# Performance work log

Measured on AMD Instinct MI355X. Metric: run time of the kernel, lower is better.

## Reference

```python
import jax, jax.numpy as jnp
import numpy as np

TWO_PI = 2.0 * np.pi
PC_RANGE = (-140.8, -40.0, -3.0, 140.8, 40.0, 1.0)
IOU_THR = 0.1
EPS = 1e-5


def limit_period(val):
    # maps angle to [-pi, pi)
    return val - jnp.floor(val / TWO_PI + 0.5) * TWO_PI


def _cross(u, v):
    return u[..., 0] * v[..., 1] - u[..., 1] * v[..., 0]


def corners_bev(boxes):
    # boxes: [N,7] = (x, y, z, h, w, l, yaw)  (order 'hwl')
    tmpl = jnp.array([[0.5, 0.5], [0.5, -0.5], [-0.5, -0.5], [-0.5, 0.5]], dtype=boxes.dtype)
    lw = jnp.stack([boxes[:, 5], boxes[:, 4]], axis=-1)  # (l, w)
    pts = tmpl[None] * lw[:, None, :]                     # [N,4,2] local frame
    c = jnp.cos(boxes[:, 6])[:, None]
    s = jnp.sin(boxes[:, 6])[:, None]
    gx = pts[..., 0] * c - pts[..., 1] * s + boxes[:, 0:1]
    gy = pts[..., 0] * s + pts[..., 1] * c + boxes[:, 1:2]
    return jnp.stack([gx, gy], axis=-1)                   # [N,4,2]


def rect_inter_area(corners):
    # pairwise rotated-rectangle intersection area via convex-polygon candidate points
    n = corners.shape[0]
    A = corners[:, None]                                  # [N,1,4,2]
    B = corners[None, :]                                  # [1,N,4,2]
    A2 = jnp.roll(corners, -1, axis=1)[:, None]
    B2 = jnp.roll(corners, -1, axis=1)[None, :]
    a1 = A[:, :, :, None, :]
    d1 = (A2 - A)[:, :, :, None, :]
    b1 = B[:, :, None, :, :]
    d2 = (B2 - B)[:, :, None, :, :]
    den = _cross(d1, d2)                                  # [N,N,4,4]
    den_s = jnp.where(jnp.abs(den) > 1e-8, den, 1e-8)
    t = _cross(b1 - a1, d2) / den_s
    u = _cross(b1 - a1, d1) / den_s
    ok = (jnp.abs(den) > 1e-8) & (t >= 0) & (t <= 1) & (u >= 0) & (u <= 1)
    pint = (a1 + t[..., None] * d1).reshape(n, n, 16, 2)  # edge-edge intersections
    ok = ok.reshape(n, n, 16)
    Ab = jnp.broadcast_to(A, (n, n, 4, 2))
    Bb = jnp.broadcast_to(B, (n, n, 4, 2))
    A2b = jnp.broadcast_to(A2, (n, n, 4, 2))
    B2b = jnp.broadcast_to(B2, (n, n, 4, 2))

    def in_quad(p, q, qn):
        c = _cross(qn[..., None, :, :] - q[..., None, :, :], p[..., :, None, :] - q[..., None, :, :])
        return jnp.all(c <= EPS, -1) | jnp.all(c >= -EPS, -1)

    a_in_b = in_quad(Ab, Bb, B2b)
    b_in_a = in_quad(Bb, Ab, A2b)
    cand = jnp.concatenate([pint, Ab, Bb], axis=2)        # [N,N,24,2]
    m = jnp.concatenate([ok, a_in_b, b_in_a], axis=2)     # [N,N,24]
    cntf = m.sum(-1).astype(cand.dtype)
    cen = (cand * m[..., None]).sum(2) / jnp.maximum(cntf, 1.0)[..., None]
    rel = jnp.where(m[..., None], cand - cen[..., None, :], 0.0)
    ang = jnp.where(m, jnp.arctan2(rel[..., 1], rel[..., 0]), 1e9)
    idx = jnp.argsort(ang, axis=-1)
    rel_s = jnp.take_along_axis(rel, idx[..., None], axis=2)
    m_s = jnp.take_along_axis(m, idx, axis=2)
    rel_s = jnp.where(m_s[..., None], rel_s, rel_s[..., 0:1, :])  # pad with first valid point
    area = 0.5 * jnp.abs(_cross(rel_s, jnp.roll(rel_s, -1, axis=2)).sum(-1))
    return jnp.where(cntf >= 3.0, area, 0.0)


def boxes_iou3d(boxes):
    inter_bev = rect_inter_area(corners_bev(boxes))
    z, h = boxes[:, 2], boxes[:, 3]
    top = z + h / 2
    bot = z - h / 2
    oh = jnp.maximum(jnp.minimum(top[:, None], top[None, :]) - jnp.maximum(bot[:, None], bot[None, :]), 0.0)
    inter = inter_bev * oh
    vol = boxes[:, 3] * boxes[:, 4] * boxes[:, 5]
    return inter / jnp.maximum(vol[:, None] + vol[None, :] - inter, 1e-6)


def clustering(ious):
    # sequential connected-component style clustering exactly as the torch while-loop
    n = ious.shape[0]

    def cond(st):
        return jnp.any(st[0] == 0)

    def body(st):
        ci, cid = st
        idx = jnp.argmax(ci == 0)  # first unassigned box
        ci = jnp.where(ious[idx] > IOU_THR, cid, ci)
        return (ci, cid + 1)

    ci, _ = jax.lax.while_loop(cond, body, (jnp.zeros(n, jnp.int32), jnp.int32(1)))
    return ci


def cluster_fusion(boxes, scores, cids):
    n = boxes.shape[0]
    ns = n + 1  # cluster ids are 1..n; segment 0 unused
    seg_sum = lambda x: jax.ops.segment_sum(x, cids, num_segments=ns)
    cnt = seg_sum(jnp.ones(n, boxes.dtype))
    smax = jax.ops.segment_max(scores, cids, num_segments=ns)
    is_max = scores == smax[cids]
    dirs = boxes[:, 6]
    dref = jax.ops.segment_max(jnp.where(is_max, dirs, -1e9), cids, num_segments=ns)[cids]
    diff = jnp.abs(dirs - dref)
    diff = jnp.where(diff > np.pi, TWO_PI - diff, diff)
    gt = diff > np.pi / 2
    s_lt = seg_sum(jnp.where(gt, scores, 0.0))
    s_le = seg_sum(jnp.where(gt, 0.0, scores))
    keep_major = (s_lt <= s_le)[cids]
    flip = jnp.where(keep_major, gt, ~gt)
    dirs = limit_period(dirs + np.pi * flip.astype(dirs.dtype))
    sn = scores / seg_sum(scores)[cids]
    theta = jnp.arctan2(seg_sum(jnp.sin(dirs) * sn), seg_sum(jnp.cos(dirs) * sn))
    cdim = jax.ops.segment_sum(boxes[:, :6] * sn[:, None], cids, num_segments=ns)
    boxes_f = jnp.concatenate([cdim, theta[:, None]], axis=-1)[1:]
    valid = cnt[1:] > 0
    scores_f = jnp.where(valid, smax[1:], 0.0)
    boxes_f = jnp.where(valid[:, None], boxes_f, 0.0)
    return boxes_f, scores_f, valid


def range_mask(boxes_f):
    c = corners_bev(boxes_f)
    inb = ((c[..., 0] > PC_RANGE[0]) & (c[..., 0] < PC_RANGE[3]) &
           (c[..., 1] > PC_RANGE[1]) & (c[..., 1] < PC_RANGE[4]))
    return jnp.all(inb, axis=-1)


def setup_inputs() -> dict:
    key = jax.random.key(0)
    ks = jax.random.split(key, 8)
    M, D = 128, 4  # 128 objects seen by ~4 agents -> clusters of ~4
    x = jax.random.uniform(ks[0], (M,), minval=-90.0, maxval=90.0)
    y = jax.random.uniform(ks[1], (M,), minval=-30.0, maxval=30.0)
    z = jax.random.uniform(ks[2], (M,), minval=-2.2, maxval=-0.8)
    h = jax.random.uniform(ks[3], (M,), minval=1.4, maxval=1.9)
    w = jax.random.uniform(ks[4], (M,), minval=1.6, maxval=2.2)
    l = jax.random.uniform(ks[5], (M,), minval=3.5, maxval=5.0)
    yaw = jax.random.uniform(ks[6], (M,), minval=-np.pi, maxval=np.pi)
    base = jnp.stack([x, y, z, h, w, l, yaw], axis=-1)
    boxes = jnp.tile(base, (D, 1))
    noise = jax.random.normal(ks[7], (M * D, 7)) * jnp.array([0.3, 0.3, 0.1, 0.05, 0.05, 0.1, 0.05])
    boxes = (boxes + noise).astype(jnp.float32)
    scores = jax.random.uniform(jax.random.fold_in(key, 1), (M * D,), minval=0.1, maxval=1.0).astype(jnp.float32)
    return {"det_boxes": boxes, "det_scores": scores, "feat_h": 100, "feat_w": 352}


def reference(det_boxes, det_scores, feat_h, feat_w):
    boxes = det_boxes.at[:, 6].set(limit_period(det_boxes[:, 6]))
    ious = boxes_iou3d(boxes)
    cids = clustering(ious)
    boxes_f, scores_f, valid = cluster_fusion(boxes, det_scores, cids)
    valid = valid & range_mask(boxes_f)
    boxes_f = jnp.where(valid[:, None], boxes_f, 0.0)
    scores_f = jnp.where(valid, scores_f, 0.0)
    # get_roi_from_box
    gh = (PC_RANGE[4] - PC_RANGE[1]) / feat_h
    gw = (PC_RANGE[3] - PC_RANGE[0]) / feat_w
    gcx = (boxes_f[:, 0] - PC_RANGE[0]) / gw
    gcy = (boxes_f[:, 1] - PC_RANGE[1]) / gh
    gox = boxes_f[:, 5] / 2.0 / gw  # enlarge_ratio = 1
    goy = boxes_f[:, 4] / 2.0 / gh + 1.0
    xmin = jnp.maximum(gcx - gox, 0.0)
    xmax = jnp.minimum(gcx + gox, feat_w - 1.0)
    ymin = jnp.maximum(gcy - goy, 0.0)
    ymax = jnp.minimum(gcy + goy, feat_h - 1.0)
    roi = jnp.stack([xmin, xmax, ymin, ymax], axis=-1).astype(jnp.int32)
    roi = jnp.where(valid[:, None], roi, 0)
    return boxes_f, scores_f, valid, roi
```

## Files before the change

### kernel.cpp

```cpp
#include <hip/hip_runtime.h>

#define N 512
#define ADJW (N/64)
#define MAXC 64
typedef unsigned long long ull;

__device__ __forceinline__ float limit_period_f(float v){
    const float TWO_PI_F = 6.2831853071795864769f;
    return v - floorf(v/TWO_PI_F + 0.5f)*TWO_PI_F;
}

__device__ __forceinline__ unsigned fkey(float f){
    unsigned u = __float_as_uint(f);
    return (u & 0x80000000u) ? ~u : (u | 0x80000000u);
}
__device__ __forceinline__ float fdec(unsigned k){
    unsigned u = (k & 0x80000000u) ? (k ^ 0x80000000u) : ~k;
    return __uint_as_float(u);
}

__global__ __launch_bounds__(512) void adj_kernel(const float* __restrict__ boxes,
                                                  ull* __restrict__ adj){
    int i = blockIdx.x;
    int t = threadIdx.x;
    int l = t & 63, wv = t >> 6;
    int h  = l >> 5;
    int sl = l & 31;
    int hb = wv*2 + h;

    __shared__ int      s_wcnt[8];
    __shared__ int      s_list[MAXC];
    __shared__ unsigned s_row[ADJW*2];
    __shared__ float    s_boxes[N][7];
    __shared__ float    s_px[16][24], s_py[16][24], s_ang[16][24];
    __shared__ float    s_rx[16][24], s_ry[16][24], s_tm[16][24];

    if(t < ADJW*2) s_row[t] = 0u;

    float bi0=boxes[i*7+0], bi1=boxes[i*7+1], bi2=boxes[i*7+2], bi3=boxes[i*7+3],
          bi4=boxes[i*7+4], bi5=boxes[i*7+5], bi6=boxes[i*7+6];
    int j = t;
    float bj0=boxes[j*7+0], bj1=boxes[j*7+1], bj2=boxes[j*7+2], bj3=boxes[j*7+3],
          bj4=boxes[j*7+4], bj5=boxes[j*7+5], bj6=boxes[j*7+6];
    s_boxes[t][0]=bj0; s_boxes[t][1]=bj1; s_boxes[t][2]=bj2; s_boxes[t][3]=bj3;
    s_boxes[t][4]=bj4; s_boxes[t][5]=bj5; s_boxes[t][6]=bj6;

    float topi = bi2 + bi3*0.5f, boti = bi2 - bi3*0.5f;
    float topj = bj2 + bj3*0.5f, botj = bj2 - bj3*0.5f;
    float ohc = fminf(topi, topj) - fmaxf(boti, botj);
    float dx = bi0 - bj0, dy = bi1 - bj1;
    float ra = 0.5f*sqrtf(bi5*bi5 + bi4*bi4);
    float rb = 0.5f*sqrtf(bj5*bj5 + bj4*bj4);
    float rr = ra + rb + 0.01f;
    bool cand = (dx*dx + dy*dy <= rr*rr) && (ohc > 0.0f);

    ull m = __ballot(cand);
    if(l == 0) s_wcnt[wv] = __popcll(m);
    int prefix = __popcll(m & ((1ull<<l) - 1ull));
    __syncthreads();
    int base = 0, C = 0;
    #pragma unroll
    for(int k=0;k<8;++k){ int c = s_wcnt[k]; if(k < wv) base += c; C += c; }
    if(cand){
        int pos = base + prefix;
        if(pos < MAXC) s_list[pos] = j;
    }
    if(C > MAXC) C = MAXC;
    __syncthreads();

    float voli = bi3*bi4*bi5;
    const float tx[4] = {0.5f, 0.5f, -0.5f, -0.5f};
    const float ty[4] = {0.5f, -0.5f, -0.5f, 0.5f};
    float yawi = limit_period_f(bi6);
    float cA = cosf(yawi), sA = sinf(yawi);
    float axv[4], ayv[4];
    #pragma unroll
    for(int k=0;k<4;++k){
        float px = tx[k]*bi5, py = ty[k]*bi4;
        axv[k] = px*cA - py*sA + bi0;
        ayv[k] = px*sA + py*cA + bi1;
    }

    for(int k = hb; k < C; k += 16){
        int jj = s_list[k];
        float cj0=s_boxes[jj][0], cj1=s_boxes[jj][1], cj2=s_boxes[jj][2],
              cj3=s_boxes[jj][3], cj4=s_boxes[jj][4], cj5=s_boxes[jj][5],
              cj6=s_boxes[jj][6];
        float volj = cj3*cj4*cj5;
        float topj2 = cj2 + cj3*0.5f, botj2 = cj2 - cj3*0.5f;
        float oh = fminf(topi, topj2) - fmaxf(boti, botj2);
        float yawj = limit_period_f(cj6);
        float cB = cosf(yawj), sB = sinf(yawj);
        float bxv[4], byv[4];
        #pragma unroll
        for(int kk=0;kk<4;++kk){
            float qx = tx[kk]*cj5, qy = ty[kk]*cj4;
            bxv[kk] = qx*cB - qy*sB + cj0;
            byv[kk] = qx*sB + qy*cB + cj1;
        }

        const float EPSQ = 1e-5f;
        bool valid = false;
        float px = 0.f, py = 0.f;
        if(sl < 16){
            int e1 = sl >> 2, e2 = sl & 3;
            float a1x=axv[e1], a1y=ayv[e1];
            float d1x=axv[(e1+1)&3]-a1x, d1y=ayv[(e1+1)&3]-a1y;
            float b1x=bxv[e2], b1y=byv[e2];
            float d2x=bxv[(e2+1)&3]-b1x, d2y=byv[(e2+1)&3]-b1y;
            float den = d1x*d2y - d1y*d2x;
            bool okd = fabsf(den) > 1e-8f;
            float dens = okd ? den : 1e-8f;
            float wx = b1x-a1x, wy = b1y-a1y;
            float tt = (wx*d2y - wy*d2x)/dens;
            float uu = (wx*d1y - wy*d1x)/dens;
            valid = okd && (tt>=0.f) && (tt<=1.f) && (uu>=0.f) && (uu<=1.f);
            px = a1x + tt*d1x;
            py = a1y + tt*d1y;
        } else if(sl < 20){
            int kk = sl - 16;
            px = axv[kk]; py = ayv[kk];
            bool le=true, ge=true;
            #pragma unroll
            for(int e=0;e<4;++e){
                float qx=bxv[e], qy=byv[e];
                float ux=bxv[(e+1)&3]-qx, uy=byv[(e+1)&3]-qy;
                float cc = ux*(py-qy) - uy*(px-qx);
                le = le && (cc <= EPSQ);
                ge = ge && (cc >= -EPSQ);
            }
            valid = le || ge;
        } else if(sl < 24){
            int kk = sl - 20;
            px = bxv[kk]; py = byv[kk];
            bool le=true, ge=true;
            #pragma unroll
            for(int e=0;e<4;++e){
                float qx=axv[e], qy=ayv[e];
                float ux=axv[(e+1)&3]-qx, uy=ayv[(e+1)&3]-qy;
                float cc = ux*(py-qy) - uy*(px-qx);
                le = le && (cc <= EPSQ);
                ge = ge && (cc >= -EPSQ);
            }
            valid = le || ge;
        }

        ull bm = __ballot(valid);
        unsigned mh = (unsigned)(bm >> (h*32)) & 0xFFFFFFu;
        int c = __popc(mh);
        float cntf = (float)c;

        if(sl < 24){
            s_px[hb][sl] = valid ? px : 0.f;
            s_py[hb][sl] = valid ? py : 0.f;
        }
        asm volatile("s_waitcnt lgkmcnt(0)" ::: "memory");
        float sx = 0.f, sy = 0.f;
        if(sl == 0){
            #pragma unroll
            for(int kk=0;kk<24;++kk){ sx += s_px[hb][kk]; sy += s_py[hb][kk]; }
        }
        sx = __shfl(sx, l & 32);
        sy = __shfl(sy, l & 32);
        float denomc = fmaxf(cntf, 1.f);
        float cenx = sx/denomc, ceny = sy/denomc;

        float relx = valid ? (px - cenx) : 0.f;
        float rely = valid ? (py - ceny) : 0.f;
        float ang  = valid ? atan2f(rely, relx) : 1e9f;

        if(sl < 24) s_ang[hb][sl] = ang;
        asm volatile("s_waitcnt lgkmcnt(0)" ::: "memory");
        int r = 0;
        if(sl < 24){
            #pragma unroll
            for(int qq=0; qq<24; ++qq){
                float aq = s_ang[hb][qq];
                if(aq < ang) r++;
                else if(aq == ang && qq < sl) r++;
            }
        }

        if(sl < 24){
            s_rx[hb][r] = relx;
            s_ry[hb][r] = rely;
        }
        asm volatile("s_waitcnt lgkmcnt(0)" ::: "memory");
        if(sl < 24){
            int nxt = (r+1 < c) ? (r+1) : 0;
            float nx = s_rx[hb][nxt], ny = s_ry[hb][nxt];
            float tm = (r < c) ? (relx*ny - rely*nx) : 0.f;
            s_tm[hb][r] = tm;
        }
        asm volatile("s_waitcnt lgkmcnt(0)" ::: "memory");

        if(sl == 0){
            float acc = 0.f;
            #pragma unroll
            for(int kk=0;kk<24;++kk) acc += s_tm[hb][kk];
            float area = 0.5f*fabsf(acc);
            float inter_bev = (cntf >= 3.f) ? area : 0.f;
            float inter = inter_bev * oh;
            float iou = inter / fmaxf(voli+volj-inter, 1e-6f);
            if(iou > 0.1f) atomicOr(&s_row[jj>>5], 1u << (jj&31));
        }
    }
    __syncthreads();
    if(t < ADJW) adj[i*ADJW + t] = ((ull*)s_row)[t];
}

__global__ __launch_bounds__(64) void cluster_kernel(const ull* __restrict__ adj,
                                                     int* __restrict__ ci){
    int l = threadIdx.x;
    __shared__ ull s_adj[N*ADJW];
    #pragma unroll
    for(int k=0;k<64;++k) s_adj[k*64 + l] = adj[k*64 + l];
    __syncthreads();
    const unsigned char* ab = (const unsigned char*)s_adj;

    ull cov[8] = {0,0,0,0,0,0,0,0};
    int mc[8]  = {0,0,0,0,0,0,0,0};
    int cid = 1;
    #pragma unroll
    for(int g=0; g<8; ++g){
        ull cg = cov[g];
        while(~cg != 0ull){
            int b = (int)__ffsll(~cg) - 1;
            int seed = g*64 + b;
            unsigned myb = (unsigned)ab[seed*64 + l];
            #pragma unroll
            for(int k=0;k<8;++k) cov[k] |= s_adj[seed*8 + k];
            #pragma unroll
            for(int q=0;q<8;++q){ if((myb>>q)&1u) mc[q] = cid; }
            cid++;
            cg = cov[g];
        }
    }
    #pragma unroll
    for(int q=0;q<8;++q) ci[l*8+q] = mc[q];
}

__global__ __launch_bounds__(512) void fuse_kernel(
        const float* __restrict__ boxes,
        const float* __restrict__ scores,
        const int* __restrict__ ci_g,
        const int* __restrict__ fhp,
        const int* __restrict__ fwp,
        float* __restrict__ out){
    const float PI_F      = 3.14159265358979323846f;
    const float HALF_PI_F = 1.57079632679489662f;
    const float TWO_PI_F  = 6.2831853071795864769f;
    int t = threadIdx.x;

    __shared__ int      s_cnt[N];
    __shared__ unsigned s_smaxk[N];
    __shared__ unsigned s_drefk[N];
    __shared__ float    s_ssum[N];
    __shared__ float    s_slt[N], s_sle[N];
    __shared__ float    s_acc[8][N];

    float b0=boxes[t*7+0], b1=boxes[t*7+1], b2=boxes[t*7+2], b3=boxes[t*7+3],
          b4=boxes[t*7+4], b5=boxes[t*7+5], b6=boxes[t*7+6];
    float dir = limit_period_f(b6);
    float sc  = scores[t];
    int ow = ci_g[t] - 1;
    s_cnt[t] = 0;
    s_smaxk[t] = fkey(-1e30f);
    s_drefk[t] = fkey(-1e9f);
    s_ssum[t] = 0.f;
    s_slt[t] = 0.f;
    s_sle[t] = 0.f;
    #pragma unroll
    for(int k=0;k<8;++k) s_acc[k][t] = 0.f;
    __syncthreads();

    atomicAdd(&s_cnt[ow], 1);
    atomicMax(&s_smaxk[ow], fkey(sc));
    atomicAdd(&s_ssum[ow], sc);
    __syncthreads();

    float smax_b = fdec(s_smaxk[ow]);
    if(sc == smax_b) atomicMax(&s_drefk[ow], fkey(dir));
    __syncthreads();

    float drefb = fdec(s_drefk[ow]);
    float diff = fabsf(dir - drefb);
    diff = (diff > PI_F) ? (TWO_PI_F - diff) : diff;
    bool gt = diff > HALF_PI_F;
    atomicAdd(gt ? &s_slt[ow] : &s_sle[ow], sc);
    __syncthreads();

    {
        bool keep = (s_slt[ow] <= s_sle[ow]);
        bool flip = keep ? gt : !gt;
        float d2 = limit_period_f(dir + (flip ? PI_F : 0.f));
        float sn = sc / s_ssum[ow];
        atomicAdd(&s_acc[0][ow], sinf(d2)*sn);
        atomicAdd(&s_acc[1][ow], cosf(d2)*sn);
        atomicAdd(&s_acc[2][ow], b0*sn);
        atomicAdd(&s_acc[3][ow], b1*sn);
        atomicAdd(&s_acc[4][ow], b2*sn);
        atomicAdd(&s_acc[5][ow], b3*sn);
        atomicAdd(&s_acc[6][ow], b4*sn);
        atomicAdd(&s_acc[7][ow], b5*sn);
    }
    __syncthreads();

    int icnt = s_cnt[t];
    float smax = fdec(s_smaxk[t]);
    float theta = atan2f(s_acc[0][t], s_acc[1][t]);
    bool valid = icnt > 0;
    float bf[7];
    bf[0] = valid ? s_acc[2][t] : 0.f;
    bf[1] = valid ? s_acc[3][t] : 0.f;
    bf[2] = valid ? s_acc[4][t] : 0.f;
    bf[3] = valid ? s_acc[5][t] : 0.f;
    bf[4] = valid ? s_acc[6][t] : 0.f;
    bf[5] = valid ? s_acc[7][t] : 0.f;
    bf[6] = valid ? theta : 0.f;
    {
        float cth=cosf(bf[6]), sth=sinf(bf[6]);
        const float tx[4]={0.5f,0.5f,-0.5f,-0.5f};
        const float ty[4]={0.5f,-0.5f,-0.5f,0.5f};
        bool inb = true;
        #pragma unroll
        for(int k=0;k<4;++k){
            float pxl = tx[k]*bf[5], pyl = ty[k]*bf[4];
            float gx = pxl*cth - pyl*sth + bf[0];
            float gy = pxl*sth + pyl*cth + bf[1];
            inb = inb && (gx > -140.8f) && (gx < 140.8f) && (gy > -40.0f) && (gy < 40.0f);
        }
        valid = valid && inb;
    }
    if(!valid){
        #pragma unroll
        for(int d=0;d<7;++d) bf[d]=0.f;
    }
    float sf = valid ? smax : 0.f;
    int fh = *fhp, fw = *fwp;
    float ghf = (float)((40.0 - (-40.0)) / (double)fh);
    float gwf = (float)((140.8 - (-140.8)) / (double)fw);
    float gcx = (bf[0] + 140.8f) / gwf;
    float gcy = (bf[1] + 40.0f) / ghf;
    float gox = bf[5]*0.5f / gwf;
    float goy = bf[4]*0.5f / ghf + 1.0f;
    float xmin = fmaxf(gcx - gox, 0.f);
    float xmax = fminf(gcx + gox, (float)fw - 1.0f);
    float ymin = fmaxf(gcy - goy, 0.f);
    float ymax = fminf(gcy + goy, (float)fh - 1.0f);
    int r0 = (int)xmin, r1 = (int)xmax, r2 = (int)ymin, r3 = (int)ymax;
    if(!valid){ r0=0; r1=0; r2=0; r3=0; }
    #pragma unroll
    for(int d=0;d<7;++d) out[t*7+d] = bf[d];
    out[N*7 + t] = sf;
    out[N*8 + t] = valid ? 1.f : 0.f;
    out[N*9 + t*4 + 0] = (float)r0;
    out[N*9 + t*4 + 1] = (float)r1;
    out[N*9 + t*4 + 2] = (float)r2;
    out[N*9 + t*4 + 3] = (float)r3;
}

extern "C" void kernel_launch(void* const* d_in, const int* in_sizes, int n_in,
                              void* d_out, int out_size, void* d_ws, size_t ws_size,
                              hipStream_t stream) {
    const float* boxes  = (const float*)d_in[0];
    const float* scores = (const float*)d_in[1];
    const int*   fhp    = (const int*)d_in[2];
    const int*   fwp    = (const int*)d_in[3];
    float* out = (float*)d_out;
    char* ws = (char*)d_ws;
    ull* adj = (ull*)ws;
    int* ci  = (int*)(ws + 32768);

    adj_kernel<<<N, 512, 0, stream>>>(boxes, adj);
    cluster_kernel<<<1, 64, 0, stream>>>(adj, ci);
    fuse_kernel<<<1, 512, 0, stream>>>(boxes, scores, ci, fhp, fwp, out);
}
```

Measured before the change: 39.08 us.

## Fuse adjacency, clustering and fusion kernels into one cooperative kernel

Replaces three kernel launches with a single cooperative kernel of 256 blocks. Each block loops over rows to build the IoU adjacency matrix, then a grid-wide sync hands off to block 0, which runs clustering and fusion from shared memory. Each block also stages all boxes in shared memory once instead of reading them per row. The aim is to remove launch gaps and the global round-trip of cluster ids, at the cost of grid-sync overhead and half as many blocks for the adjacency work.

```diff
diff --git a/kernel.cpp b/kernel.cpp
--- a/kernel.cpp
+++ b/kernel.cpp
@@ -1,4 +1,6 @@
 #include <hip/hip_runtime.h>
+#include <hip/hip_cooperative_groups.h>
+namespace cg = cooperative_groups;
 
 #define N 512
 #define ADJW (N/64)
@@ -9,7 +11,6 @@
     const float TWO_PI_F = 6.2831853071795864769f;
     return v - floorf(v/TWO_PI_F + 0.5f)*TWO_PI_F;
 }
-
 __device__ __forceinline__ unsigned fkey(float f){
     unsigned u = __float_as_uint(f);
     return (u & 0x80000000u) ? ~u : (u | 0x80000000u);
@@ -19,251 +20,262 @@
     return __uint_as_float(u);
 }
 
-__global__ __launch_bounds__(512) void adj_kernel(const float* __restrict__ boxes,
-                                                  ull* __restrict__ adj){
-    int i = blockIdx.x;
+__global__ __launch_bounds__(512, 4) void mega_kernel(
+        const float* __restrict__ boxes,
+        const float* __restrict__ scores,
+        const int* __restrict__ fhp,
+        const int* __restrict__ fwp,
+        ull* __restrict__ adj,
+        float* __restrict__ out){
+    const float PI_F      = 3.14159265358979323846f;
+    const float HALF_PI_F = 1.57079632679489662f;
+    const float TWO_PI_F  = 6.2831853071795864769f;
     int t = threadIdx.x;
     int l = t & 63, wv = t >> 6;
     int h  = l >> 5;
     int sl = l & 31;
     int hb = wv*2 + h;
 
-    __shared__ int      s_wcnt[8];
-    __shared__ int      s_list[MAXC];
-    __shared__ unsigned s_row[ADJW*2];
-    __shared__ float    s_boxes[N][7];
-    __shared__ float    s_px[16][24], s_py[16][24], s_ang[16][24];
-    __shared__ float    s_rx[16][24], s_ry[16][24], s_tm[16][24];
-
-    if(t < ADJW*2) s_row[t] = 0u;
-
-    float bi0=boxes[i*7+0], bi1=boxes[i*7+1], bi2=boxes[i*7+2], bi3=boxes[i*7+3],
-          bi4=boxes[i*7+4], bi5=boxes[i*7+5], bi6=boxes[i*7+6];
-    int j = t;
-    float bj0=boxes[j*7+0], bj1=boxes[j*7+1], bj2=boxes[j*7+2], bj3=boxes[j*7+3],
-          bj4=boxes[j*7+4], bj5=boxes[j*7+5], bj6=boxes[j*7+6];
-    s_boxes[t][0]=bj0; s_boxes[t][1]=bj1; s_boxes[t][2]=bj2; s_boxes[t][3]=bj3;
-    s_boxes[t][4]=bj4; s_boxes[t][5]=bj5; s_boxes[t][6]=bj6;
-
-    float topi = bi2 + bi3*0.5f, boti = bi2 - bi3*0.5f;
-    float topj = bj2 + bj3*0.5f, botj = bj2 - bj3*0.5f;
-    float ohc = fminf(topi, topj) - fmaxf(boti, botj);
-    float dx = bi0 - bj0, dy = bi1 - bj1;
-    float ra = 0.5f*sqrtf(bi5*bi5 + bi4*bi4);
-    float rb = 0.5f*sqrtf(bj5*bj5 + bj4*bj4);
-    float rr = ra + rb + 0.01f;
-    bool cand = (dx*dx + dy*dy <= rr*rr) && (ohc > 0.0f);
-
-    ull m = __ballot(cand);
-    if(l == 0) s_wcnt[wv] = __popcll(m);
-    int prefix = __popcll(m & ((1ull<<l) - 1ull));
-    __syncthreads();
-    int base = 0, C = 0;
+    __shared__ __align__(16) char s_raw[34816];
+    float (*s_boxes)[7] = (float(*)[7])s_raw;
+    int*      p_list = (int*)(s_raw + 14336);
+    unsigned* p_row  = (unsigned*)(s_raw + 14592);
+    int*      p_wcnt = (int*)(s_raw + 14656);
+    float* p_px  = (float*)(s_raw + 14720);
+    float* p_py  = p_px  + 16*24;
+    float* p_ang = p_py  + 16*24;
+    float* p_rx  = p_ang + 16*24;
+    float* p_ry  = p_rx  + 16*24;
+    float* p_tm  = p_ry  + 16*24;
+
     #pragma unroll
-    for(int k=0;k<8;++k){ int c = s_wcnt[k]; if(k < wv) base += c; C += c; }
-    if(cand){
-        int pos = base + prefix;
-        if(pos < MAXC) s_list[pos] = j;
-    }
-    if(C > MAXC) C = MAXC;
-    __syncthreads();
-
-    float voli = bi3*bi4*bi5;
+    for(int d=0; d<7; ++d) s_boxes[t][d] = boxes[t*7+d];
+    __syncthreads();
+
     const float tx[4] = {0.5f, 0.5f, -0.5f, -0.5f};
     const float ty[4] = {0.5f, -0.5f, -0.5f, 0.5f};
-    float yawi = limit_period_f(bi6);
-    float cA = cosf(yawi), sA = sinf(yawi);
-    float axv[4], ayv[4];
+
+    for(int row = blockIdx.x; row < N; row += gridDim.x){
+        __syncthreads();
+        if(t < ADJW*2) p_row[t] = 0u;
+
+        float bi0=s_boxes[row][0], bi1=s_boxes[row][1], bi2=s_boxes[row][2],
+              bi3=s_boxes[row][3], bi4=s_boxes[row][4], bi5=s_boxes[row][5],
+              bi6=s_boxes[row][6];
+        int j = t;
+        float bj0=s_boxes[j][0], bj1=s_boxes[j][1], bj2=s_boxes[j][2],
+              bj3=s_boxes[j][3], bj4=s_boxes[j][4], bj5=s_boxes[j][5];
+
+        float topi = bi2 + bi3*0.5f, boti = bi2 - bi3*0.5f;
+        float topj = bj2 + bj3*0.5f, botj = bj2 - bj3*0.5f;
+        float ohc = fminf(topi, topj) - fmaxf(boti, botj);
+        float dx = bi0 - bj0, dy = bi1 - bj1;
+        float ra = 0.5f*sqrtf(bi5*bi5 + bi4*bi4);
+        float rb = 0.5f*sqrtf(bj5*bj5 + bj4*bj4);
+        float rr = ra + rb + 0.01f;
+        bool cand = (dx*dx + dy*dy <= rr*rr) && (ohc > 0.0f);
+
+        ull m = __ballot(cand);
+        if(l == 0) p_wcnt[wv] = __popcll(m);
+        int prefix = __popcll(m & ((1ull<<l) - 1ull));
+        __syncthreads();
+        int base = 0, C = 0;
+        #pragma unroll
+        for(int k=0;k<8;++k){ int c = p_wcnt[k]; if(k < wv) base += c; C += c; }
+        if(cand){
+            int pos = base + prefix;
+            if(pos < MAXC) p_list[pos] = j;
+        }
+        if(C > MAXC) C = MAXC;
+        __syncthreads();
+
+        float voli = bi3*bi4*bi5;
+        float yawi = limit_period_f(bi6);
+        float cA = cosf(yawi), sA = sinf(yawi);
+        float axv[4], ayv[4];
+        #pragma unroll
+        for(int k=0;k<4;++k){
+            float px = tx[k]*bi5, py = ty[k]*bi4;
+            axv[k] = px*cA - py*sA + bi0;
+            ayv[k] = px*sA + py*cA + bi1;
+        }
+
+        for(int k = hb; k < C; k += 16){
+            int jj = p_list[k];
+            float cj0=s_boxes[jj][0], cj1=s_boxes[jj][1], cj2=s_boxes[jj][2],
+                  cj3=s_boxes[jj][3], cj4=s_boxes[jj][4], cj5=s_boxes[jj][5],
+                  cj6=s_boxes[jj][6];
+            float volj = cj3*cj4*cj5;
+            float topj2 = cj2 + cj3*0.5f, botj2 = cj2 - cj3*0.5f;
+            float oh = fminf(topi, topj2) - fmaxf(boti, botj2);
+            float yawj = limit_period_f(cj6);
+            float cB = cosf(yawj), sB = sinf(yawj);
+            float bxv[4], byv[4];
+            #pragma unroll
+            for(int kk=0;kk<4;++kk){
+                float qx = tx[kk]*cj5, qy = ty[kk]*cj4;
+                bxv[kk] = qx*cB - qy*sB + cj0;
+                byv[kk] = qx*sB + qy*cB + cj1;
+            }
+
+            const float EPSQ = 1e-5f;
+            bool valid = false;
+            float px = 0.f, py = 0.f;
+            if(sl < 16){
+                int e1 = sl >> 2, e2 = sl & 3;
+                float a1x=axv[e1], a1y=ayv[e1];
+                float d1x=axv[(e1+1)&3]-a1x, d1y=ayv[(e1+1)&3]-a1y;
+                float b1x=bxv[e2], b1y=byv[e2];
+                float d2x=bxv[(e2+1)&3]-b1x, d2y=byv[(e2+1)&3]-b1y;
+                float den = d1x*d2y - d1y*d2x;
+                bool okd = fabsf(den) > 1e-8f;
+                float dens = okd ? den : 1e-8f;
+                float wx = b1x-a1x, wy = b1y-a1y;
+                float tt = (wx*d2y - wy*d2x)/dens;
+                float uu = (wx*d1y - wy*d1x)/dens;
+                valid = okd && (tt>=0.f) && (tt<=1.f) && (uu>=0.f) && (uu<=1.f);
+                px = a1x + tt*d1x;
+                py = a1y + tt*d1y;
+            } else if(sl < 20){
+                int kk = sl - 16;
+                px = axv[kk]; py = ayv[kk];
+                bool le=true, ge=true;
+                #pragma unroll
+                for(int e=0;e<4;++e){
+                    float qx=bxv[e], qy=byv[e];
+                    float ux=bxv[(e+1)&3]-qx, uy=byv[(e+1)&3]-qy;
+                    float cc = ux*(py-qy) - uy*(px-qx);
+                    le = le && (cc <= EPSQ);
+                    ge = ge && (cc >= -EPSQ);
+                }
+                valid = le || ge;
+            } else if(sl < 24){
+                int kk = sl - 20;
+                px = bxv[kk]; py = byv[kk];
+                bool le=true, ge=true;
+                #pragma unroll
+                for(int e=0;e<4;++e){
+                    float qx=axv[e], qy=ayv[e];
+                    float ux=axv[(e+1)&3]-qx, uy=ayv[(e+1)&3]-qy;
+                    float cc = ux*(py-qy) - uy*(px-qx);
+                    le = le && (cc <= EPSQ);
+                    ge = ge && (cc >= -EPSQ);
+                }
+                valid = le || ge;
+            }
+
+            ull bm = __ballot(valid);
+            unsigned mh = (unsigned)(bm >> (h*32)) & 0xFFFFFFu;
+            int c = __popc(mh);
+            float cntf = (float)c;
+
+            if(sl < 24){
+                p_px[hb*24+sl] = valid ? px : 0.f;
+                p_py[hb*24+sl] = valid ? py : 0.f;
+            }
+            asm volatile("s_waitcnt lgkmcnt(0)" ::: "memory");
+            float sx = 0.f, sy = 0.f;
+            if(sl == 0){
+                #pragma unroll
+                for(int kk=0;kk<24;++kk){ sx += p_px[hb*24+kk]; sy += p_py[hb*24+kk]; }
+            }
+            sx = __shfl(sx, l & 32);
+            sy = __shfl(sy, l & 32);
+            float denomc = fmaxf(cntf, 1.f);
+            float cenx = sx/denomc, ceny = sy/denomc;
+
+            float relx = valid ? (px - cenx) : 0.f;
+            float rely = valid ? (py - ceny) : 0.f;
+            float ang  = valid ? atan2f(rely, relx) : 1e9f;
+
+            if(sl < 24) p_ang[hb*24+sl] = ang;
+            asm volatile("s_waitcnt lgkmcnt(0)" ::: "memory");
+            int r = 0;
+            if(sl < 24){
+                #pragma unroll
+                for(int qq=0; qq<24; ++qq){
+                    float aq = p_ang[hb*24+qq];
+                    if(aq < ang) r++;
+                    else if(aq == ang && qq < sl) r++;
+                }
+            }
+
+            if(sl < 24){
+                p_rx[hb*24+r] = relx;
+                p_ry[hb*24+r] = rely;
+            }
+            asm volatile("s_waitcnt lgkmcnt(0)" ::: "memory");
+            if(sl < 24){
+                int nxt = (r+1 < c) ? (r+1) : 0;
+                float nx = p_rx[hb*24+nxt], ny = p_ry[hb*24+nxt];
+                float tm = (r < c) ? (relx*ny - rely*nx) : 0.f;
+                p_tm[hb*24+r] = tm;
+            }
+            asm volatile("s_waitcnt lgkmcnt(0)" ::: "memory");
+
+            if(sl == 0){
+                float acc = 0.f;
+                #pragma unroll
+                for(int kk=0;kk<24;++kk) acc += p_tm[hb*24+kk];
+                float area = 0.5f*fabsf(acc);
+                float inter_bev = (cntf >= 3.f) ? area : 0.f;
+                float inter = inter_bev * oh;
+                float iou = inter / fmaxf(voli+volj-inter, 1e-6f);
+                if(iou > 0.1f) atomicOr(&p_row[jj>>5], 1u << (jj&31));
+            }
+        }
+        __syncthreads();
+        if(t < ADJW) adj[row*ADJW + t] = ((ull*)p_row)[t];
+    }
+
+    __threadfence();
+    cg::this_grid().sync();
+    if(blockIdx.x != 0) return;
+
+    ull* s_adj = (ull*)s_raw;
+    int* s_ci  = (int*)(s_raw + 32768);
     #pragma unroll
-    for(int k=0;k<4;++k){
-        float px = tx[k]*bi5, py = ty[k]*bi4;
-        axv[k] = px*cA - py*sA + bi0;
-        ayv[k] = px*sA + py*cA + bi1;
-    }
-
-    for(int k = hb; k < C; k += 16){
-        int jj = s_list[k];
-        float cj0=s_boxes[jj][0], cj1=s_boxes[jj][1], cj2=s_boxes[jj][2],
-              cj3=s_boxes[jj][3], cj4=s_boxes[jj][4], cj5=s_boxes[jj][5],
-              cj6=s_boxes[jj][6];
-        float volj = cj3*cj4*cj5;
-        float topj2 = cj2 + cj3*0.5f, botj2 = cj2 - cj3*0.5f;
-        float oh = fminf(topi, topj2) - fmaxf(boti, botj2);
-        float yawj = limit_period_f(cj6);
-        float cB = cosf(yawj), sB = sinf(yawj);
-        float bxv[4], byv[4];
-        #pragma unroll
-        for(int kk=0;kk<4;++kk){
-            float qx = tx[kk]*cj5, qy = ty[kk]*cj4;
-            bxv[kk] = qx*cB - qy*sB + cj0;
-            byv[kk] = qx*sB + qy*cB + cj1;
-        }
-
-        const float EPSQ = 1e-5f;
-        bool valid = false;
-        float px = 0.f, py = 0.f;
-        if(sl < 16){
-            int e1 = sl >> 2, e2 = sl & 3;
-            float a1x=axv[e1], a1y=ayv[e1];
-            float d1x=axv[(e1+1)&3]-a1x, d1y=ayv[(e1+1)&3]-a1y;
-            float b1x=bxv[e2], b1y=byv[e2];
-            float d2x=bxv[(e2+1)&3]-b1x, d2y=byv[(e2+1)&3]-b1y;
-            float den = d1x*d2y - d1y*d2x;
-            bool okd = fabsf(den) > 1e-8f;
-            float dens = okd ? den : 1e-8f;
-            float wx = b1x-a1x, wy = b1y-a1y;
-            float tt = (wx*d2y - wy*d2x)/dens;
-            float uu = (wx*d1y - wy*d1x)/dens;
-            valid = okd && (tt>=0.f) && (tt<=1.f) && (uu>=0.f) && (uu<=1.f);
-            px = a1x + tt*d1x;
-            py = a1y + tt*d1y;
-        } else if(sl < 20){
-            int kk = sl - 16;
-            px = axv[kk]; py = ayv[kk];
-            bool le=true, ge=true;
-            #pragma unroll
-            for(int e=0;e<4;++e){
-                float qx=bxv[e], qy=byv[e];
-                float ux=bxv[(e+1)&3]-qx, uy=byv[(e+1)&3]-qy;
-                float cc = ux*(py-qy) - uy*(px-qx);
-                le = le && (cc <= EPSQ);
-                ge = ge && (cc >= -EPSQ);
-            }
-            valid = le || ge;
-        } else if(sl < 24){
-            int kk = sl - 20;
-            px = bxv[kk]; py = byv[kk];
-            bool le=true, ge=true;
-            #pragma unroll
-            for(int e=0;e<4;++e){
-                float qx=axv[e], qy=ayv[e];
-                float ux=axv[(e+1)&3]-qx, uy=ayv[(e+1)&3]-qy;
-                float cc = ux*(py-qy) - uy*(px-qx);
-                le = le && (cc <= EPSQ);
-                ge = ge && (cc >= -EPSQ);
-            }
-            valid = le || ge;
-        }
-
-        ull bm = __ballot(valid);
-        unsigned mh = (unsigned)(bm >> (h*32)) & 0xFFFFFFu;
-        int c = __popc(mh);
-        float cntf = (float)c;
-
-        if(sl < 24){
-            s_px[hb][sl] = valid ? px : 0.f;
-            s_py[hb][sl] = valid ? py : 0.f;
-        }
-        asm volatile("s_waitcnt lgkmcnt(0)" ::: "memory");
-        float sx = 0.f, sy = 0.f;
-        if(sl == 0){
-            #pragma unroll
-            for(int kk=0;kk<24;++kk){ sx += s_px[hb][kk]; sy += s_py[hb][kk]; }
-        }
-        sx = __shfl(sx, l & 32);
-        sy = __shfl(sy, l & 32);
-        float denomc = fmaxf(cntf, 1.f);
-        float cenx = sx/denomc, ceny = sy/denomc;
-
-        float relx = valid ? (px - cenx) : 0.f;
-        float rely = valid ? (py - ceny) : 0.f;
-        float ang  = valid ? atan2f(rely, relx) : 1e9f;
-
-        if(sl < 24) s_ang[hb][sl] = ang;
-        asm volatile("s_waitcnt lgkmcnt(0)" ::: "memory");
-        int r = 0;
-        if(sl < 24){
-            #pragma unroll
-            for(int qq=0; qq<24; ++qq){
-                float aq = s_ang[hb][qq];
-                if(aq < ang) r++;
-                else if(aq == ang && qq < sl) r++;
-            }
-        }
-
-        if(sl < 24){
-            s_rx[hb][r] = relx;
-            s_ry[hb][r] = rely;
-        }
-        asm volatile("s_waitcnt lgkmcnt(0)" ::: "memory");
-        if(sl < 24){
-            int nxt = (r+1 < c) ? (r+1) : 0;
-            float nx = s_rx[hb][nxt], ny = s_ry[hb][nxt];
-            float tm = (r < c) ? (relx*ny - rely*nx) : 0.f;
-            s_tm[hb][r] = tm;
-        }
-        asm volatile("s_waitcnt lgkmcnt(0)" ::: "memory");
-
-        if(sl == 0){
-            float acc = 0.f;
-            #pragma unroll
-            for(int kk=0;kk<24;++kk) acc += s_tm[hb][kk];
-            float area = 0.5f*fabsf(acc);
-            float inter_bev = (cntf >= 3.f) ? area : 0.f;
-            float inter = inter_bev * oh;
-            float iou = inter / fmaxf(voli+volj-inter, 1e-6f);
-            if(iou > 0.1f) atomicOr(&s_row[jj>>5], 1u << (jj&31));
-        }
-    }
-    __syncthreads();
-    if(t < ADJW) adj[i*ADJW + t] = ((ull*)s_row)[t];
-}
-
-__global__ __launch_bounds__(64) void cluster_kernel(const ull* __restrict__ adj,
-                                                     int* __restrict__ ci){
-    int l = threadIdx.x;
-    __shared__ ull s_adj[N*ADJW];
-    #pragma unroll
-    for(int k=0;k<64;++k) s_adj[k*64 + l] = adj[k*64 + l];
-    __syncthreads();
-    const unsigned char* ab = (const unsigned char*)s_adj;
-
-    ull cov[8] = {0,0,0,0,0,0,0,0};
-    int mc[8]  = {0,0,0,0,0,0,0,0};
-    int cid = 1;
-    #pragma unroll
-    for(int g=0; g<8; ++g){
-        ull cg = cov[g];
-        while(~cg != 0ull){
-            int b = (int)__ffsll(~cg) - 1;
-            int seed = g*64 + b;
-            unsigned myb = (unsigned)ab[seed*64 + l];
-            #pragma unroll
-            for(int k=0;k<8;++k) cov[k] |= s_adj[seed*8 + k];
-            #pragma unroll
-            for(int q=0;q<8;++q){ if((myb>>q)&1u) mc[q] = cid; }
-            cid++;
-            cg = cov[g];
-        }
-    }
-    #pragma unroll
-    for(int q=0;q<8;++q) ci[l*8+q] = mc[q];
-}
-
-__global__ __launch_bounds__(512) void fuse_kernel(
-        const float* __restrict__ boxes,
-        const float* __restrict__ scores,
-        const int* __restrict__ ci_g,
-        const int* __restrict__ fhp,
-        const int* __restrict__ fwp,
-        float* __restrict__ out){
-    const float PI_F      = 3.14159265358979323846f;
-    const float HALF_PI_F = 1.57079632679489662f;
-    const float TWO_PI_F  = 6.2831853071795864769f;
-    int t = threadIdx.x;
-
-    __shared__ int      s_cnt[N];
-    __shared__ unsigned s_smaxk[N];
-    __shared__ unsigned s_drefk[N];
-    __shared__ float    s_ssum[N];
-    __shared__ float    s_slt[N], s_sle[N];
-    __shared__ float    s_acc[8][N];
-
+    for(int k=0;k<ADJW;++k) s_adj[k*N + t] = adj[k*N + t];
+    __syncthreads();
+
+    if(t < 64){
+        const unsigned char* ab = (const unsigned char*)s_adj;
+        ull cov[8] = {0,0,0,0,0,0,0,0};
+        int mc[8]  = {0,0,0,0,0,0,0,0};
+        int cid = 1;
+        #pragma unroll
+        for(int g=0; g<8; ++g){
+            ull cg2 = cov[g];
+            while(~cg2 != 0ull){
+                int b = (int)__ffsll(~cg2) - 1;
+                int seed = g*64 + b;
+                unsigned myb = (unsigned)ab[seed*64 + t];
+                #pragma unroll
+                for(int k=0;k<8;++k) cov[k] |= s_adj[seed*8 + k];
+                #pragma unroll
+                for(int q=0;q<8;++q){ if((myb>>q)&1u) mc[q] = cid; }
+                cid++;
+                cg2 = cov[g];
+            }
+        }
+        #pragma unroll
+        for(int q=0;q<8;++q) s_ci[t*8+q] = mc[q];
+    }
+    __syncthreads();
+
+    int ow = s_ci[t] - 1;
     float b0=boxes[t*7+0], b1=boxes[t*7+1], b2=boxes[t*7+2], b3=boxes[t*7+3],
           b4=boxes[t*7+4], b5=boxes[t*7+5], b6=boxes[t*7+6];
     float dir = limit_period_f(b6);
     float sc  = scores[t];
-    int ow = ci_g[t] - 1;
+
+    int*      s_cnt   = (int*)s_raw;
+    unsigned* s_smaxk = (unsigned*)(s_raw + 2048);
+    unsigned* s_drefk = (unsigned*)(s_raw + 4096);
+    float*    s_ssum  = (float*)(s_raw + 6144);
+    float*    s_slt   = (float*)(s_raw + 8192);
+    float*    s_sle   = (float*)(s_raw + 10240);
+    float*    s_acc   = (float*)(s_raw + 12288);
     s_cnt[t] = 0;
     s_smaxk[t] = fkey(-1e30f);
     s_drefk[t] = fkey(-1e9f);
@@ -271,7 +283,7 @@
     s_slt[t] = 0.f;
     s_sle[t] = 0.f;
     #pragma unroll
-    for(int k=0;k<8;++k) s_acc[k][t] = 0.f;
+    for(int k=0;k<8;++k) s_acc[k*N + t] = 0.f;
     __syncthreads();
 
     atomicAdd(&s_cnt[ow], 1);
@@ -295,33 +307,31 @@
         bool flip = keep ? gt : !gt;
         float d2 = limit_period_f(dir + (flip ? PI_F : 0.f));
         float sn = sc / s_ssum[ow];
-        atomicAdd(&s_acc[0][ow], sinf(d2)*sn);
-        atomicAdd(&s_acc[1][ow], cosf(d2)*sn);
-        atomicAdd(&s_acc[2][ow], b0*sn);
-        atomicAdd(&s_acc[3][ow], b1*sn);
-        atomicAdd(&s_acc[4][ow], b2*sn);
-        atomicAdd(&s_acc[5][ow], b3*sn);
-        atomicAdd(&s_acc[6][ow], b4*sn);
-        atomicAdd(&s_acc[7][ow], b5*sn);
+        atomicAdd(&s_acc[0*N+ow], sinf(d2)*sn);
+        atomicAdd(&s_acc[1*N+ow], cosf(d2)*sn);
+        atomicAdd(&s_acc[2*N+ow], b0*sn);
+        atomicAdd(&s_acc[3*N+ow], b1*sn);
+        atomicAdd(&s_acc[4*N+ow], b2*sn);
+        atomicAdd(&s_acc[5*N+ow], b3*sn);
+        atomicAdd(&s_acc[6*N+ow], b4*sn);
+        atomicAdd(&s_acc[7*N+ow], b5*sn);
     }
     __syncthreads();
 
     int icnt = s_cnt[t];
     float smax = fdec(s_smaxk[t]);
-    float theta = atan2f(s_acc[0][t], s_acc[1][t]);
+    float theta = atan2f(s_acc[0*N+t], s_acc[1*N+t]);
     bool valid = icnt > 0;
     float bf[7];
-    bf[0] = valid ? s_acc[2][t] : 0.f;
-    bf[1] = valid ? s_acc[3][t] : 0.f;
-    bf[2] = valid ? s_acc[4][t] : 0.f;
-    bf[3] = valid ? s_acc[5][t] : 0.f;
-    bf[4] = valid ? s_acc[6][t] : 0.f;
-    bf[5] = valid ? s_acc[7][t] : 0.f;
+    bf[0] = valid ? s_acc[2*N+t] : 0.f;
+    bf[1] = valid ? s_acc[3*N+t] : 0.f;
+    bf[2] = valid ? s_acc[4*N+t] : 0.f;
+    bf[3] = valid ? s_acc[5*N+t] : 0.f;
+    bf[4] = valid ? s_acc[6*N+t] : 0.f;
+    bf[5] = valid ? s_acc[7*N+t] : 0.f;
     bf[6] = valid ? theta : 0.f;
     {
         float cth=cosf(bf[6]), sth=sinf(bf[6]);
-        const float tx[4]={0.5f,0.5f,-0.5f,-0.5f};
-        const float ty[4]={0.5f,-0.5f,-0.5f,0.5f};
         bool inb = true;
         #pragma unroll
         for(int k=0;k<4;++k){
@@ -368,11 +378,15 @@
     const int*   fhp    = (const int*)d_in[2];
     const int*   fwp    = (const int*)d_in[3];
     float* out = (float*)d_out;
-    char* ws = (char*)d_ws;
-    ull* adj = (ull*)ws;
-    int* ci  = (int*)(ws + 32768);
-
-    adj_kernel<<<N, 512, 0, stream>>>(boxes, adj);
-    cluster_kernel<<<1, 64, 0, stream>>>(adj, ci);
-    fuse_kernel<<<1, 512, 0, stream>>>(boxes, scores, ci, fhp, fwp, out);
-}
+    ull* adj = (ull*)d_ws;
+
+    void* args[6];
+    args[0] = (void*)&boxes;
+    args[1] = (void*)&scores;
+    args[2] = (void*)&fhp;
+    args[3] = (void*)&fwp;
+    args[4] = (void*)&adj;
+    args[5] = (void*)&out;
+    hipLaunchCooperativeKernel((const void*)mega_kernel, dim3(256), dim3(512),
+                               args, 0, stream);
+}
```

New measurement: 122.0 us. +212.1%, slower.
